# Optimization experiments

Measured on AMD Instinct MI355X. Metric: run time of the kernel, lower is better.

## Reference

```python
import jax, jax.numpy as jnp
import numpy as np

N = 4096      # nnode
F = 128       # feature_dim
E = 64        # embed_dim
P_EDGE = 0.01 # edge probability (~41 avg degree)
NEG = -9e15
ALPHA = 0.2   # leaky relu slope


def _xavier(key, shape):
    lim = float(np.sqrt(6.0 / (shape[0] + shape[1])))
    return jax.random.uniform(key, shape, minval=-lim, maxval=lim, dtype=jnp.float32)


def setup_inputs() -> dict:
    key = jax.random.key(0)
    ks = jax.random.split(key, 14)
    features = jax.random.normal(ks[0], (N, F), dtype=jnp.float32)
    eye = jnp.eye(N, dtype=jnp.float32)

    def make_adj(k):
        a = (jax.random.uniform(k, (N, N)) < P_EDGE).astype(jnp.float32)
        return jnp.maximum(a, eye)  # self loop so no empty rows

    return {
        "features": features,
        "geo_adj": make_adj(ks[1]),
        "forward_adj": make_adj(ks[2]),
        "backward_adj": make_adj(ks[3]),
        "weight": _xavier(ks[4], (E, F)),
        "Wf": _xavier(ks[5], (F, E)),
        "af1": jax.random.normal(ks[6], (E,), dtype=jnp.float32) * 0.1,
        "af2": jax.random.normal(ks[7], (E,), dtype=jnp.float32) * 0.1,
        "Wb": _xavier(ks[8], (F, E)),
        "ab1": jax.random.normal(ks[9], (E,), dtype=jnp.float32) * 0.1,
        "ab2": jax.random.normal(ks[10], (E,), dtype=jnp.float32) * 0.1,
        "Wg": _xavier(ks[11], (F, E)),
        "ag1": jax.random.normal(ks[12], (E,), dtype=jnp.float32) * 0.1,
        "ag2": jax.random.normal(ks[13], (E,), dtype=jnp.float32) * 0.1,
    }


def _mean_neighbors(adj, feat):
    # pre_weight: row-normalized neighbor averaging, (N,N) @ (N,F)
    deg = jnp.clip(jnp.sum(adj, axis=1, keepdims=True), 1.0, None)
    return (adj @ feat) / deg


def _attention(feat, mask_feat, adj, W, a1, a2):
    # GAT-style additive attention with masked softmax over neighbors
    h = feat @ W        # (N, E)
    hm = mask_feat @ W  # (N, E)
    e = jax.nn.leaky_relu((h @ a1)[:, None] + (hm @ a2)[None, :], negative_slope=ALPHA)  # (N, N)
    e = jnp.where(adj > 0, e, NEG)
    return jax.nn.softmax(e, axis=1)  # (N, N)


def reference(features, geo_adj, forward_adj, backward_adj, weight,
              Wf, af1, af2, Wb, ab1, ab2, Wg, ag1, ag2):
    t = features  # (N, F)
    mask_f = _mean_neighbors(forward_adj, t)
    mask_b = _mean_neighbors(backward_adj, t)
    mask_g = _mean_neighbors(geo_adj, t)

    w_f = _attention(t, mask_f, forward_adj, Wf, af1, af2)
    w_b = _attention(t, mask_b, backward_adj, Wb, ab1, ab2)
    w_g = _attention(t, mask_g, geo_adj, Wg, ag1, ag2)

    # get_mask_matrix_i/_j broadcast-mul + sum(1) == attn @ t (or attn.T @ t)
    x = weight @ t.T                  # (E, N)
    x_fwd = weight @ (w_f @ t).T      # mask_matrix_i
    x_bwd = weight @ (w_b.T @ t).T    # mask_matrix_j (transposed)
    x_geo = weight @ (w_g @ t).T      # mask_matrix_i

    return jnp.concatenate([x, x_fwd, x_bwd, x_geo], axis=0)  # (4E, N)
```

## Files before the change

### kernel.cpp

```cpp
#include <hip/hip_runtime.h>

#define NN 4096
#define FF 128
#define EE 64

typedef unsigned short u16;

__device__ __forceinline__ float lrelu(float x) { return x > 0.f ? x : 0.2f * x; }

__global__ void k_prep(const float* __restrict__ Wf, const float* __restrict__ af1, const float* __restrict__ af2,
                       const float* __restrict__ Wb, const float* __restrict__ ab1, const float* __restrict__ ab2,
                       const float* __restrict__ Wg, const float* __restrict__ ag1, const float* __restrict__ ag2,
                       float* __restrict__ v6)
{
    const float* Ws[3]  = {Wf, Wb, Wg};
    const float* a1s[3] = {af1, ab1, ag1};
    const float* a2s[3] = {af2, ab2, ag2};
    int tid = threadIdx.x;
    for (int idx = tid; idx < 6 * FF; idx += 256) {
        int vi = idx >> 7, f = idx & (FF - 1), dd = vi >> 1;
        const float* a = (vi & 1) ? a2s[dd] : a1s[dd];
        const float* W = Ws[dd];
        float s = 0.f;
        for (int e = 0; e < EE; ++e) s += W[(size_t)f * EE + e] * a[e];
        v6[idx] = s;
    }
}

__global__ void k_feat(const float* __restrict__ t, const float* __restrict__ weight,
                       const float* __restrict__ v6,
                       float* __restrict__ u, float* __restrict__ s1, float* __restrict__ p,
                       float* __restrict__ out, int* __restrict__ ccnt)
{
    __shared__ __attribute__((aligned(16))) float tt[FF];
    __shared__ float vv[6 * FF];
    int n = blockIdx.x, tid = threadIdx.x;
    if (n < 16) ccnt[n * 256 + tid] = 0;
    if (tid < FF) tt[tid] = t[(size_t)n * FF + tid];
    for (int idx = tid; idx < 6 * FF; idx += 256) vv[idx] = v6[idx];
    __syncthreads();
    int e = tid >> 2, part = tid & 3;
    const float4* w4 = reinterpret_cast<const float4*>(weight + (size_t)e * FF + part * 32);
    const float4* t4 = reinterpret_cast<const float4*>(tt + part * 32);
    float s = 0.f;
    #pragma unroll
    for (int q8 = 0; q8 < 8; ++q8) {
        float4 w = w4[q8]; float4 x = t4[q8];
        s += w.x * x.x + w.y * x.y + w.z * x.z + w.w * x.w;
    }
    s += __shfl_xor(s, 1); s += __shfl_xor(s, 2);
    if (part == 0) {
        u[(size_t)n * EE + e] = s;
        out[(size_t)e * NN + n] = s;
    }
    if (tid < 64) {
        float t0 = tt[tid], t1 = tt[64 + tid];
        for (int vi = 0; vi < 6; ++vi) {
            float x = t0 * vv[vi * FF + tid] + t1 * vv[vi * FF + 64 + tid];
            for (int off = 32; off; off >>= 1) x += __shfl_xor(x, off);
            if (tid == 0) {
                int dd = vi >> 1;
                if (vi & 1) p[dd * NN + n] = x; else s1[dd * NN + n] = x;
            }
        }
    }
}

__global__ void k_scan(const float* __restrict__ Af, const float* __restrict__ Ab, const float* __restrict__ Ag,
                       u16* __restrict__ csr, int* __restrict__ cnt,
                       u16* __restrict__ csc, int* __restrict__ ccnt, int stride)
{
    __shared__ int wcnt[4];
    int gr = blockIdx.x;
    int d = gr >> 12, r = gr & (NN - 1);
    const float* A = d == 0 ? Af : (d == 1 ? Ab : Ag);
    const float4* row4 = reinterpret_cast<const float4*>(A + (size_t)r * NN);
    int tid = threadIdx.x, wave = tid >> 6, lane = tid & 63;

    float4 L0 = row4[tid];
    float4 L1 = row4[256 + tid];
    float4 L2 = row4[512 + tid];
    float4 L3 = row4[768 + tid];
    float vals[16] = {L0.x, L0.y, L0.z, L0.w, L1.x, L1.y, L1.z, L1.w,
                      L2.x, L2.y, L2.z, L2.w, L3.x, L3.y, L3.z, L3.w};
    int lc = 0;
    #pragma unroll
    for (int k = 0; k < 16; ++k) lc += (vals[k] != 0.f) ? 1 : 0;

    int sc = lc;
    for (int off = 1; off < 64; off <<= 1) {
        int o = __shfl_up(sc, off);
        if (lane >= off) sc += o;
    }
    if (lane == 63) wcnt[wave] = sc;
    __syncthreads();
    int prefix = 0, total = 0;
    #pragma unroll
    for (int w = 0; w < 4; ++w) {
        int c = wcnt[w];
        if (w < wave) prefix += c;
        total += c;
    }
    int pos = prefix + sc - lc;
    u16* crow = csr + (size_t)gr * stride;
    #pragma unroll
    for (int k = 0; k < 4; ++k)
        #pragma unroll
        for (int m = 0; m < 4; ++m)
            if (vals[k * 4 + m] != 0.f) {
                if (pos < stride) crow[pos] = (u16)(k * 1024 + tid * 4 + m);
                pos++;
            }
    if (d == 1) {
        #pragma unroll
        for (int k = 0; k < 4; ++k)
            #pragma unroll
            for (int m = 0; m < 4; ++m)
                if (vals[k * 4 + m] != 0.f) {
                    int col = k * 1024 + tid * 4 + m;
                    int cp = atomicAdd(&ccnt[col], 1);
                    if (cp < stride) csc[(size_t)col * stride + cp] = (u16)r;
                }
    }
    if (tid == 0) cnt[gr] = total;
}

__global__ void k_q(const float* __restrict__ p, const u16* __restrict__ csr,
                    const int* __restrict__ cnt, int stride, float* __restrict__ s2)
{
    int tid = threadIdx.x, wave = tid >> 6, lane = tid & 63;
    int gr = blockIdx.x * 4 + wave;
    int d = gr >> 12;
    int nnz = min(cnt[gr], stride);
    const u16* crow = csr + (size_t)gr * stride;
    const float* pd = p + d * NN;
    float q = 0.f;
    if (lane < nnz)      q += pd[crow[lane]];
    if (lane + 64 < nnz) q += pd[crow[lane + 64]];
    for (int off = 32; off; off >>= 1) q += __shfl_xor(q, off);
    if (lane == 0) s2[gr] = q / fmaxf((float)nnz, 1.f);
}

__global__ void k_zb(const float* __restrict__ s1, const float* __restrict__ s2,
                     const u16* __restrict__ csr, const int* __restrict__ cnt, int stride,
                     float* __restrict__ Zb)
{
    int tid = threadIdx.x, wave = tid >> 6, lane = tid & 63;
    int j = blockIdx.x * 4 + wave;
    int gr = NN + j;
    int nnz = min(cnt[gr], stride);
    const u16* crow = csr + (size_t)gr * stride;
    float s1j = s1[gr];
    const float* s2b = s2 + NN;
    float z = 0.f;
    if (lane < nnz)      z += __expf(lrelu(s1j + s2b[crow[lane]]));
    if (lane + 64 < nnz) z += __expf(lrelu(s1j + s2b[crow[lane + 64]]));
    for (int off = 32; off; off >>= 1) z += __shfl_xor(z, off);
    if (lane == 0) Zb[j] = z;
}

__global__ void k_out(const float* __restrict__ u,
                      const float* __restrict__ s1, const float* __restrict__ s2,
                      const float* __restrict__ Zb,
                      const u16* __restrict__ csr, const int* __restrict__ cnt,
                      const u16* __restrict__ csc, const int* __restrict__ ccnt, int stride,
                      float* __restrict__ out)
{
    __shared__ float wl[128]; __shared__ int il[128];
    __shared__ float zsum; __shared__ float oacc[4 * EE];
    int gr = blockIdx.x;
    int d = gr >> 12, i = gr & (NN - 1);
    int tid = threadIdx.x, wave = tid >> 6, lane = tid & 63;
    if (tid == 0) zsum = 0.f;
    __syncthreads();
    float invz;
    int nnz;
    if (d == 1) {
        nnz = min(ccnt[i], stride);
        const u16* ccol = csc + (size_t)i * stride;
        float s2i = s2[NN + i];
        if (tid < nnz) {
            int j = ccol[tid];
            il[tid] = j;
            wl[tid] = __expf(lrelu(s1[NN + j] + s2i)) / Zb[j];
        }
        invz = 1.f;
        __syncthreads();
    } else {
        nnz = min(cnt[gr], stride);
        const u16* crow = csr + (size_t)gr * stride;
        float s1i = s1[gr];
        const float* s2d = s2 + d * NN;
        float z = 0.f;
        if (tid < nnz) {
            int col = crow[tid];
            float w = __expf(lrelu(s1i + s2d[col]));
            il[tid] = col; wl[tid] = w; z = w;
        }
        for (int off = 32; off; off >>= 1) z += __shfl_xor(z, off);
        if (lane == 0) atomicAdd(&zsum, z);
        __syncthreads();
        float zs = zsum;
        invz = zs > 0.f ? 1.f / zs : 0.f;
    }
    float a0 = 0.f, a1 = 0.f;
    int k = wave;
    for (; k + 4 < nnz; k += 8) {
        a0 += wl[k]     * u[(size_t)il[k]     * EE + lane];
        a1 += wl[k + 4] * u[(size_t)il[k + 4] * EE + lane];
    }
    for (; k < nnz; k += 4)
        a0 += wl[k] * u[(size_t)il[k] * EE + lane];
    oacc[wave * EE + lane] = a0 + a1;
    __syncthreads();
    if (wave == 0) {
        float rsum = (oacc[lane] + oacc[EE + lane] + oacc[2 * EE + lane] + oacc[3 * EE + lane]) * invz;
        int base = 64 + (d << 6);
        out[(size_t)(base + lane) * NN + i] = rsum;
    }
}

extern "C" void kernel_launch(void* const* d_in, const int* in_sizes, int n_in,
                              void* d_out, int out_size, void* d_ws, size_t ws_size,
                              hipStream_t stream)
{
    const float* t   = (const float*)d_in[0];
    const float* Ag  = (const float*)d_in[1];
    const float* Af  = (const float*)d_in[2];
    const float* Ab  = (const float*)d_in[3];
    const float* W   = (const float*)d_in[4];
    const float* Wf  = (const float*)d_in[5];
    const float* af1 = (const float*)d_in[6];
    const float* af2 = (const float*)d_in[7];
    const float* Wb  = (const float*)d_in[8];
    const float* ab1 = (const float*)d_in[9];
    const float* ab2 = (const float*)d_in[10];
    const float* Wg  = (const float*)d_in[11];
    const float* ag1 = (const float*)d_in[12];
    const float* ag2 = (const float*)d_in[13];
    float* out = (float*)d_out;

    float* ws = (float*)d_ws;
    float* v6  = ws;
    float* s1  = v6 + 6 * FF;
    float* p   = s1 + 3 * NN;
    float* s2  = p + 3 * NN;
    float* Zb  = s2 + 3 * NN;
    float* u   = Zb + NN;
    int*   cnt  = (int*)(u + (size_t)NN * EE);
    int*   ccnt = cnt + 3 * NN;
    u16*   csr  = (u16*)(ccnt + NN);

    size_t base_bytes = ((char*)csr) - ((char*)d_ws);
    int stride = 128;
    if (base_bytes + (size_t)4 * NN * 128 * 2 > ws_size) stride = 96;
    if (base_bytes + (size_t)4 * NN * 96 * 2 > ws_size)  stride = 64;
    u16* csc = csr + (size_t)3 * NN * stride;

    k_prep<<<1, 256, 0, stream>>>(Wf, af1, af2, Wb, ab1, ab2, Wg, ag1, ag2, v6);
    k_feat<<<NN, 256, 0, stream>>>(t, W, v6, u, s1, p, out, ccnt);
    k_scan<<<3 * NN, 256, 0, stream>>>(Af, Ab, Ag, csr, cnt, csc, ccnt, stride);
    k_q<<<3 * NN / 4, 256, 0, stream>>>(p, csr, cnt, stride, s2);
    k_zb<<<NN / 4, 256, 0, stream>>>(s1, s2, csr, cnt, stride, Zb);
    k_out<<<3 * NN, 256, 0, stream>>>(u, s1, s2, Zb, csr, cnt, csc, ccnt, stride, out);
}
```

Before: 281.4 us.

## Fuse neighbor-score reduction into adjacency scan with wave-per-row bitmask compaction

The adjacency scan now gives each 64-lane wave its own row instead of a whole block. Each lane packs its 64 loaded values into a 64-bit nonzero bitmask, and a wave-level prefix scan replaces the shared-memory cross-wave step and the __syncthreads barrier. The separate k_q kernel is folded into the scan, so the p-gather sum and s2 are computed while the column indices are emitted. This saves a launch and a re-read of the CSR lists, and keeps more loads in flight per wave. The trade-off is that CSR entries come out in a different column order and register pressure rises from holding 16 float4 loads.

```diff
diff --git a/kernel.cpp b/kernel.cpp
--- a/kernel.cpp
+++ b/kernel.cpp
@@ -66,79 +66,64 @@
     }
 }
 
-__global__ void k_scan(const float* __restrict__ Af, const float* __restrict__ Ab, const float* __restrict__ Ag,
-                       u16* __restrict__ csr, int* __restrict__ cnt,
-                       u16* __restrict__ csc, int* __restrict__ ccnt, int stride)
-{
-    __shared__ int wcnt[4];
-    int gr = blockIdx.x;
+__global__ __launch_bounds__(256, 4)
+void k_scan(const float* __restrict__ Af, const float* __restrict__ Ab, const float* __restrict__ Ag,
+            const float* __restrict__ p,
+            u16* __restrict__ csr, int* __restrict__ cnt, float* __restrict__ s2,
+            u16* __restrict__ csc, int* __restrict__ ccnt, int stride)
+{
+    int wid = threadIdx.x >> 6, lane = threadIdx.x & 63;
+    int gr = blockIdx.x * 4 + wid;
     int d = gr >> 12, r = gr & (NN - 1);
     const float* A = d == 0 ? Af : (d == 1 ? Ab : Ag);
     const float4* row4 = reinterpret_cast<const float4*>(A + (size_t)r * NN);
-    int tid = threadIdx.x, wave = tid >> 6, lane = tid & 63;
-
-    float4 L0 = row4[tid];
-    float4 L1 = row4[256 + tid];
-    float4 L2 = row4[512 + tid];
-    float4 L3 = row4[768 + tid];
-    float vals[16] = {L0.x, L0.y, L0.z, L0.w, L1.x, L1.y, L1.z, L1.w,
-                      L2.x, L2.y, L2.z, L2.w, L3.x, L3.y, L3.z, L3.w};
-    int lc = 0;
-    #pragma unroll
-    for (int k = 0; k < 16; ++k) lc += (vals[k] != 0.f) ? 1 : 0;
-
+    const float* pd = p + d * NN;
+
+    float4 l0 = row4[lane],        l1 = row4[64 + lane],  l2 = row4[128 + lane],
+           l3 = row4[192 + lane],  l4 = row4[256 + lane], l5 = row4[320 + lane],
+           l6 = row4[384 + lane],  l7 = row4[448 + lane], l8 = row4[512 + lane],
+           l9 = row4[576 + lane],  l10 = row4[640 + lane], l11 = row4[704 + lane],
+           l12 = row4[768 + lane], l13 = row4[832 + lane], l14 = row4[896 + lane],
+           l15 = row4[960 + lane];
+
+    unsigned long long mask = 0ull;
+#define MBITS(L, J) { unsigned mm = (L.x != 0.f ? 1u : 0u) | (L.y != 0.f ? 2u : 0u) | \
+                                    (L.z != 0.f ? 4u : 0u) | (L.w != 0.f ? 8u : 0u); \
+                      mask |= ((unsigned long long)mm) << (J * 4); }
+    MBITS(l0, 0)  MBITS(l1, 1)  MBITS(l2, 2)  MBITS(l3, 3)
+    MBITS(l4, 4)  MBITS(l5, 5)  MBITS(l6, 6)  MBITS(l7, 7)
+    MBITS(l8, 8)  MBITS(l9, 9)  MBITS(l10, 10) MBITS(l11, 11)
+    MBITS(l12, 12) MBITS(l13, 13) MBITS(l14, 14) MBITS(l15, 15)
+#undef MBITS
+
+    int lc = __popcll(mask);
     int sc = lc;
     for (int off = 1; off < 64; off <<= 1) {
         int o = __shfl_up(sc, off);
         if (lane >= off) sc += o;
     }
-    if (lane == 63) wcnt[wave] = sc;
-    __syncthreads();
-    int prefix = 0, total = 0;
-    #pragma unroll
-    for (int w = 0; w < 4; ++w) {
-        int c = wcnt[w];
-        if (w < wave) prefix += c;
-        total += c;
-    }
-    int pos = prefix + sc - lc;
+    int total = __shfl(sc, 63);
+    int pos = sc - lc;
     u16* crow = csr + (size_t)gr * stride;
-    #pragma unroll
-    for (int k = 0; k < 4; ++k)
-        #pragma unroll
-        for (int m = 0; m < 4; ++m)
-            if (vals[k * 4 + m] != 0.f) {
-                if (pos < stride) crow[pos] = (u16)(k * 1024 + tid * 4 + m);
-                pos++;
-            }
-    if (d == 1) {
-        #pragma unroll
-        for (int k = 0; k < 4; ++k)
-            #pragma unroll
-            for (int m = 0; m < 4; ++m)
-                if (vals[k * 4 + m] != 0.f) {
-                    int col = k * 1024 + tid * 4 + m;
-                    int cp = atomicAdd(&ccnt[col], 1);
-                    if (cp < stride) csc[(size_t)col * stride + cp] = (u16)r;
-                }
-    }
-    if (tid == 0) cnt[gr] = total;
-}
-
-__global__ void k_q(const float* __restrict__ p, const u16* __restrict__ csr,
-                    const int* __restrict__ cnt, int stride, float* __restrict__ s2)
-{
-    int tid = threadIdx.x, wave = tid >> 6, lane = tid & 63;
-    int gr = blockIdx.x * 4 + wave;
-    int d = gr >> 12;
-    int nnz = min(cnt[gr], stride);
-    const u16* crow = csr + (size_t)gr * stride;
-    const float* pd = p + d * NN;
     float q = 0.f;
-    if (lane < nnz)      q += pd[crow[lane]];
-    if (lane + 64 < nnz) q += pd[crow[lane + 64]];
+    unsigned long long m = mask;
+    while (m) {
+        int b = __ffsll((unsigned long long)m) - 1;
+        m &= m - 1;
+        int col = ((b >> 2) << 8) + (lane << 2) + (b & 3);
+        if (pos < stride) crow[pos] = (u16)col;
+        pos++;
+        q += pd[col];
+        if (d == 1) {
+            int cp = atomicAdd(&ccnt[col], 1);
+            if (cp < stride) csc[(size_t)col * stride + cp] = (u16)r;
+        }
+    }
     for (int off = 32; off; off >>= 1) q += __shfl_xor(q, off);
-    if (lane == 0) s2[gr] = q / fmaxf((float)nnz, 1.f);
+    if (lane == 0) {
+        cnt[gr] = total;
+        s2[gr] = q / fmaxf((float)total, 1.f);
+    }
 }
 
 __global__ void k_zb(const float* __restrict__ s1, const float* __restrict__ s2,
@@ -259,8 +244,7 @@
 
     k_prep<<<1, 256, 0, stream>>>(Wf, af1, af2, Wb, ab1, ab2, Wg, ag1, ag2, v6);
     k_feat<<<NN, 256, 0, stream>>>(t, W, v6, u, s1, p, out, ccnt);
-    k_scan<<<3 * NN, 256, 0, stream>>>(Af, Ab, Ag, csr, cnt, csc, ccnt, stride);
-    k_q<<<3 * NN / 4, 256, 0, stream>>>(p, csr, cnt, stride, s2);
+    k_scan<<<3 * NN / 4, 256, 0, stream>>>(Af, Ab, Ag, p, csr, cnt, s2, csc, ccnt, stride);
     k_zb<<<NN / 4, 256, 0, stream>>>(s1, s2, csr, cnt, stride, Zb);
     k_out<<<3 * NN, 256, 0, stream>>>(u, s1, s2, Zb, csr, cnt, csc, ccnt, stride, out);
 }
```

After: 278.6 us. Within noise of the previous version (-1.0%).
